# Kernel tuning notes

Measured on AMD Instinct MI355X. Metric: run time of the kernel, lower is better.

The kernel has to match this reference:

```python
import jax, jax.numpy as jnp
import numpy as np

B, S, D, H = 4, 2048, 1024, 16
DK = D // H

def setup_inputs() -> dict:
    key = jax.random.key(0)
    ks = jax.random.split(key, 5)
    scale = D ** -0.5  # keep activations well-scaled for random weights
    return {
        "x": jax.random.normal(ks[0], (B, S, D), dtype=jnp.float32),
        "w_q": jax.random.normal(ks[1], (D, D), dtype=jnp.float32) * scale,
        "w_k": jax.random.normal(ks[2], (D, D), dtype=jnp.float32) * scale,
        "w_v": jax.random.normal(ks[3], (D, D), dtype=jnp.float32) * scale,
        "w_o": jax.random.normal(ks[4], (D, D), dtype=jnp.float32) * scale,
        "b_o": jnp.zeros((D,), dtype=jnp.float32),
    }

def reference(x, w_q, w_k, w_v, w_o, b_o):
    b, s, d = x.shape
    # nn.Linear applies x @ W^T; project then split heads -> [b, h, s, dk]
    q = (x @ w_q.T).reshape(b, s, H, DK).transpose(0, 2, 1, 3)
    k = (x @ w_k.T).reshape(b, s, H, DK).transpose(0, 2, 1, 3)
    v = (x @ w_v.T).reshape(b, s, H, DK).transpose(0, 2, 1, 3)
    scores = jnp.einsum('bhqd,bhkd->bhqk', q, k) * (DK ** -0.5)
    causal = jnp.tril(jnp.ones((s, s), dtype=bool))  # [s, s]
    scores = jnp.where(causal, scores, jnp.float32(-1e9))
    attn = jax.nn.softmax(scores, axis=-1)
    out = jnp.einsum('bhqk,bhkd->bhqd', attn, v)
    out = out.transpose(0, 2, 1, 3).reshape(b, s, d)
    return out @ w_o.T + b_o
```

## Files before the change

### kernel.cpp

```cpp
#include <hip/hip_runtime.h>

typedef unsigned short u16;
typedef unsigned int u32;
typedef __attribute__((ext_vector_type(4))) u16 u16x4;
typedef __attribute__((ext_vector_type(8))) short short8;
typedef __attribute__((ext_vector_type(4))) float f32x4;
typedef __attribute__((ext_vector_type(16))) float f32x16;
typedef __attribute__((ext_vector_type(4))) u32 uint4v;

#define AS1 __attribute__((address_space(1)))
#define AS3 __attribute__((address_space(3)))

#define B_  4
#define S_  2048
#define D_  1024
#define H_  16
#define DK_ 64

#define WAIT_VM(n) asm volatile("s_waitcnt vmcnt(" #n ")" ::: "memory")
#define WAIT_LGK0  asm volatile("s_waitcnt lgkmcnt(0)" ::: "memory")

__device__ __forceinline__ u16 f2bf(float f) {
  union { float f; unsigned u; } v; v.f = f;
  unsigned r = v.u + 0x7fffu + ((v.u >> 16) & 1u);
  return (u16)(r >> 16);
}

__device__ __forceinline__ u32 cvt_pk_bf16(float lo, float hi) {
  u32 r;
  asm("v_cvt_pk_bf16_f32 %0, %1, %2" : "=v"(r) : "v"(lo), "v"(hi));
  return r;
}

__device__ __forceinline__ void pl32_swap(u32& a, u32& b) {
  asm("v_permlane32_swap_b32 %0, %1" : "+v"(a), "+v"(b));
}

__device__ __forceinline__ void gload_lds16(const void* g, void* l) {
  __builtin_amdgcn_global_load_lds((const AS1 void*)g, (AS3 void*)l, 16, 0, 0);
}

__global__ __launch_bounds__(256) void conv_bf16(const float* __restrict__ in,
                                                 u16* __restrict__ out,
                                                 int n, float scale) {
  int i = (blockIdx.x * 256 + threadIdx.x) * 8;
  if (i >= n) return;
  f32x4 a = *reinterpret_cast<const f32x4*>(in + i);
  f32x4 b = *reinterpret_cast<const f32x4*>(in + i + 4);
  union { u16 u[8]; uint4v v; } r;
#pragma unroll
  for (int j = 0; j < 4; ++j) {
    r.u[j]     = f2bf(a[j] * scale);
    r.u[4 + j] = f2bf(b[j] * scale);
  }
  *reinterpret_cast<uint4v*>(out + i) = r.v;
}

__global__ __launch_bounds__(256) void conv_w4(const float* __restrict__ w0,
                                               const float* __restrict__ w1,
                                               const float* __restrict__ w2,
                                               const float* __restrict__ w3,
                                               u16* __restrict__ out, float s0) {
  int y = blockIdx.y;
  const float* src = (y == 0) ? w0 : (y == 1) ? w1 : (y == 2) ? w2 : w3;
  float scale = (y == 0) ? s0 : 1.0f;
  int i = (blockIdx.x * 256 + threadIdx.x) * 8;
  f32x4 a = *reinterpret_cast<const f32x4*>(src + i);
  f32x4 b = *reinterpret_cast<const f32x4*>(src + i + 4);
  union { u16 u[8]; uint4v v; } r;
#pragma unroll
  for (int j = 0; j < 4; ++j) {
    r.u[j]     = f2bf(a[j] * scale);
    r.u[4 + j] = f2bf(b[j] * scale);
  }
  *reinterpret_cast<uint4v*>(out + (size_t)y * (D_ * D_) + i) = r.v;
}

template<int MODE>
__global__ __launch_bounds__(256) void gemm_bt(const u16* __restrict__ A,
                                               const u16* __restrict__ B,
                                               u16* __restrict__ Qb,
                                               u16* __restrict__ Kb,
                                               u16* __restrict__ Vt,
                                               float* __restrict__ Cf,
                                               const float* __restrict__ bias,
                                               int M, int N, int K, int nbx) {
  __shared__ __attribute__((aligned(16))) u16 As[2][128 * 64];
  __shared__ __attribute__((aligned(16))) u16 Bs[2][128 * 64];

  const int t = threadIdx.x;
  const int l = t & 63;
  const int w = t >> 6;
  const int wr = w >> 1, wc = w & 1;
  const int dd = blockIdx.x;
  const int cpx = gridDim.x >> 3;
  const int lid = (dd & 7) * cpx + (dd >> 3);
  const int m0 = (lid / nbx) * 128;
  const int n0 = (lid % nbx) * 128;
  const int NT = K >> 6;

  f32x4 zero = {0.f, 0.f, 0.f, 0.f};
  f32x4 acc[4][4];
#pragma unroll
  for (int i = 0; i < 4; ++i)
#pragma unroll
    for (int j = 0; j < 4; ++j) acc[i][j] = zero;

  auto stage = [&](int kt, int buf) {
#pragma unroll
    for (int i = 0; i < 4; ++i) {
      int slot = i * 256 + t;
      int r = slot >> 3, c = slot & 7;
      gload_lds16(A + (size_t)(m0 + r) * K + kt * 64 + ((c ^ (r & 7)) * 8),
                  (char*)&As[buf][0] + (size_t)(i * 256 + w * 64) * 16);
      gload_lds16(B + (size_t)(n0 + r) * K + kt * 64 + ((c ^ (r & 7)) * 8),
                  (char*)&Bs[buf][0] + (size_t)(i * 256 + w * 64) * 16);
    }
  };

  stage(0, 0);
  stage(1, 1);

  for (int kt = 0; kt < NT; ++kt) {
    const int buf = kt & 1;
    if (kt < NT - 1) { WAIT_VM(8); } else { WAIT_VM(0); }
    __builtin_amdgcn_s_barrier();
    __builtin_amdgcn_sched_barrier(0);

#pragma unroll
    for (int kc = 0; kc < 2; ++kc) {
      short8 a[4], bf[4];
      int lc = kc * 4 + (l >> 4);
#pragma unroll
      for (int i = 0; i < 4; ++i) {
        int ra = wr * 64 + i * 16 + (l & 15);
        a[i] = *reinterpret_cast<const short8*>(&As[buf][ra * 64 + ((lc ^ (ra & 7)) * 8)]);
        int rb = wc * 64 + i * 16 + (l & 15);
        bf[i] = *reinterpret_cast<const short8*>(&Bs[buf][rb * 64 + ((lc ^ (rb & 7)) * 8)]);
      }
#pragma unroll
      for (int mi = 0; mi < 4; ++mi)
#pragma unroll
        for (int ni = 0; ni < 4; ++ni)
          acc[mi][ni] = __builtin_amdgcn_mfma_f32_16x16x32_bf16(a[mi], bf[ni], acc[mi][ni], 0, 0, 0);
    }

    WAIT_LGK0;
    __builtin_amdgcn_sched_barrier(0);
    __builtin_amdgcn_s_barrier();
    if (kt + 2 < NT) stage(kt + 2, buf);
  }

#pragma unroll
  for (int ni = 0; ni < 4; ++ni) {
    int col = n0 + wc * 64 + ni * 16 + (l & 15);
    float bv = (MODE == 1) ? bias[col] : 0.f;
#pragma unroll
    for (int mi = 0; mi < 4; ++mi) {
      int row0 = m0 + wr * 64 + mi * 16 + (l >> 4) * 4;
      if (MODE == 1) {
#pragma unroll
        for (int r = 0; r < 4; ++r)
          Cf[(size_t)(row0 + r) * N + col] = acc[mi][ni][r] + bv;
      } else {
        if (col < 2048) {
          u16* dst = (col < 1024) ? Qb : Kb;
          int c = col & 1023;
#pragma unroll
          for (int r = 0; r < 4; ++r)
            dst[(size_t)(row0 + r) * 1024 + c] = f2bf(acc[mi][ni][r]);
        } else {
          int vc = col - 2048;
          int bh = (row0 >> 11) * 16 + (vc >> 6);
          int s0 = row0 & 2047;
          u16x4 pk;
#pragma unroll
          for (int r = 0; r < 4; ++r) pk[r] = f2bf(acc[mi][ni][r]);
          *reinterpret_cast<u16x4*>(Vt + ((size_t)(bh * 64 + (vc & 63))) * 2048 + s0) = pk;
        }
      }
    }
  }
}

__global__ __launch_bounds__(512) void attn_fwd(const u16* __restrict__ Q,
                                                const u16* __restrict__ K,
                                                const u16* __restrict__ Vtg,
                                                u16* __restrict__ AO) {
  __shared__ __attribute__((aligned(16))) u16 smem[24576];
  u16* Ksb = smem;
  u16* Vsb = smem + 12288;

  const int t = threadIdx.x;
  const int l = t & 63;
  const int w = t >> 6;
  const int hi = l >> 5;
  const int hi8 = hi * 8, hi4 = hi * 4;
  const int bh = blockIdx.x;
  const int by = blockIdx.y;
  const int s = (by < 4) ? (7 - 2 * by) : (2 * (by - 4));
  const size_t qkbase = (size_t)((bh >> 4) * S_) * D_ + (bh & 15) * DK_;
  const u16* Vg = Vtg + (size_t)bh * 64 * S_;

  const int qw = s * 256 + w * 32;
  const int qi = qw + (l & 31);

  short8 qf[4];
#pragma unroll
  for (int c = 0; c < 4; ++c)
    qf[c] = *reinterpret_cast<const short8*>(Q + qkbase + (size_t)qi * D_ + c * 16 + hi8);

  f32x16 o0 = {0,0,0,0,0,0,0,0,0,0,0,0,0,0,0,0};
  f32x16 o1 = {0,0,0,0,0,0,0,0,0,0,0,0,0,0,0,0};
  float l_r = 0.f;

  const int nst = 4 * (s + 1);

  auto stage = [&](int jt, u16* kdst, u16* vdst) {
    const u16* Ksrc = K + qkbase + (size_t)(jt * 64) * D_;
    const u16* Vsrc = Vg + jt * 64;
    int r = t >> 3, c = t & 7;
    gload_lds16(Ksrc + (size_t)r * D_ + ((c ^ (r & 7)) * 8),
                (char*)kdst + (size_t)t * 16);
    gload_lds16(Vsrc + (size_t)r * S_ + ((c ^ (r & 7)) * 8),
                (char*)vdst + (size_t)t * 16);
  };

  stage(0, Ksb, Vsb);
  stage(1, Ksb + 4096, Vsb + 4096);
  stage(2, Ksb + 8192, Vsb + 8192);
  int o0b = 0, o1b = 4096, o2b = 8192;

  for (int it = 0; it < nst; ++it) {
    if (it < nst - 2)       { WAIT_VM(4); }
    else if (it == nst - 2) { WAIT_VM(2); }
    else                    { WAIT_VM(0); }
    __builtin_amdgcn_s_barrier();
    __builtin_amdgcn_sched_barrier(0);

    const int j0 = it * 64;
    u16* ks = Ksb + o0b;
    u16* vs = Vsb + o0b;

    if (j0 <= qw + 31) {
      f32x16 s0 = {0,0,0,0,0,0,0,0,0,0,0,0,0,0,0,0};
      f32x16 s1 = {0,0,0,0,0,0,0,0,0,0,0,0,0,0,0,0};
#pragma unroll
      for (int c = 0; c < 4; ++c) {
        int cl = 2 * c + hi;
        int k0r = l & 31, k1r = (l & 31) + 32;
        short8 kf0 = *reinterpret_cast<const short8*>(&ks[k0r * 64 + ((cl ^ (k0r & 7)) * 8)]);
        short8 kf1 = *reinterpret_cast<const short8*>(&ks[k1r * 64 + ((cl ^ (k1r & 7)) * 8)]);
        s0 = __builtin_amdgcn_mfma_f32_32x32x16_bf16(kf0, qf[c], s0, 0, 0, 0);
        s1 = __builtin_amdgcn_mfma_f32_32x32x16_bf16(kf1, qf[c], s1, 0, 0, 0);
      }
      if (j0 + 63 > qw) {
#pragma unroll
        for (int r = 0; r < 16; ++r) {
          int key = j0 + (r & 3) + 8 * (r >> 2) + hi4;
          if (key > qi) s0[r] = -INFINITY;
          if (key + 32 > qi) s1[r] = -INFINITY;
        }
      }
      {
        float sum = 0.f;
#pragma unroll
        for (int r = 0; r < 16; ++r) { s0[r] = exp2f(s0[r]); sum += s0[r]; }
#pragma unroll
        for (int r = 0; r < 16; ++r) { s1[r] = exp2f(s1[r]); sum += s1[r]; }
        sum += __shfl_xor(sum, 32);
        l_r += sum;
      }
#pragma unroll
      for (int ksl = 0; ksl < 4; ++ksl) {
        const int b = 8 * (ksl & 1);
        const f32x16& ps = (ksl < 2) ? s0 : s1;
        u32 c0 = cvt_pk_bf16(ps[b + 0], ps[b + 1]);
        u32 c1 = cvt_pk_bf16(ps[b + 2], ps[b + 3]);
        u32 c2 = cvt_pk_bf16(ps[b + 4], ps[b + 5]);
        u32 c3 = cvt_pk_bf16(ps[b + 6], ps[b + 7]);
        pl32_swap(c0, c2);
        pl32_swap(c1, c3);
        union { u32 u[4]; short8 s; } pa;
        pa.u[0] = c0; pa.u[1] = c1; pa.u[2] = c2; pa.u[3] = c3;
        int cl = 2 * ksl + hi;
        int d0r = l & 31, d1r = (l & 31) + 32;
        short8 vf0 = *reinterpret_cast<const short8*>(&vs[d0r * 64 + ((cl ^ (d0r & 7)) * 8)]);
        short8 vf1 = *reinterpret_cast<const short8*>(&vs[d1r * 64 + ((cl ^ (d1r & 7)) * 8)]);
        o0 = __builtin_amdgcn_mfma_f32_32x32x16_bf16(vf0, pa.s, o0, 0, 0, 0);
        o1 = __builtin_amdgcn_mfma_f32_32x32x16_bf16(vf1, pa.s, o1, 0, 0, 0);
      }
    }

    WAIT_LGK0;
    __builtin_amdgcn_sched_barrier(0);
    __builtin_amdgcn_s_barrier();
    if (it + 3 < nst) stage(it + 3, Ksb + o0b, Vsb + o0b);
    int tmp = o0b; o0b = o1b; o1b = o2b; o2b = tmp;
  }

  float inv = 1.0f / l_r;
  u16* Ob = smem + w * 2304;
#pragma unroll
  for (int acc = 0; acc < 2; ++acc) {
    const f32x16& oo = acc ? o1 : o0;
#pragma unroll
    for (int rp = 0; rp < 8; ++rp) {
      u32 pk = cvt_pk_bf16(oo[2 * rp] * inv, oo[2 * rp + 1] * inv);
      int d0 = ((2 * rp) & 3) + 8 * (rp >> 1) + hi4 + 32 * acc;
      *reinterpret_cast<u32*>(&Ob[(l & 31) * 72 + d0]) = pk;
    }
  }
  __syncthreads();
  int qq = l >> 1;
  int chb = (l & 1) * 4;
#pragma unroll
  for (int c2 = 0; c2 < 4; ++c2) {
    uint4v vv = *reinterpret_cast<const uint4v*>(&Ob[qq * 72 + (chb + c2) * 8]);
    *reinterpret_cast<uint4v*>(&AO[qkbase + (size_t)(qw + qq) * D_ + (chb + c2) * 8]) = vv;
  }
}

extern "C" void kernel_launch(void* const* d_in, const int* in_sizes, int n_in,
                              void* d_out, int out_size, void* d_ws, size_t ws_size,
                              hipStream_t stream) {
  const float* x  = (const float*)d_in[0];
  const float* wq = (const float*)d_in[1];
  const float* wk = (const float*)d_in[2];
  const float* wv = (const float*)d_in[3];
  const float* wo = (const float*)d_in[4];
  const float* bo = (const float*)d_in[5];
  float* out = (float*)d_out;

  char* ws = (char*)d_ws;
  u16* XB   = (u16*)(ws);
  u16* WQKV = (u16*)(ws + (size_t)(16 << 20));
  u16* WOB  = (u16*)(ws + (size_t)(22 << 20));
  u16* Qb   = (u16*)(ws + (size_t)(24 << 20));
  u16* Kb   = (u16*)(ws + (size_t)(40 << 20));
  u16* Vt   = (u16*)(ws + (size_t)(56 << 20));
  u16* AO   = (u16*)(ws + (size_t)(72 << 20));

  const int nx = B_ * S_ * D_;
  const int nw = D_ * D_;

  conv_bf16<<<nx / 2048, 256, 0, stream>>>(x, XB, nx, 1.0f);
  conv_w4<<<dim3(nw / 2048, 4), 256, 0, stream>>>(wq, wk, wv, wo, WQKV,
                                                  0.18033688011112042f);

  gemm_bt<0><<<1536, 256, 0, stream>>>(
      XB, WQKV, Qb, Kb, Vt, nullptr, nullptr, B_ * S_, 3072, D_, 24);

  attn_fwd<<<dim3(B_ * H_, 8), 512, 0, stream>>>(Qb, Kb, Vt, AO);

  gemm_bt<1><<<512, 256, 0, stream>>>(
      AO, WOB, nullptr, nullptr, nullptr, out, bo, B_ * S_, D_, D_, 8);
}
```

Measured before the change: 163.3 us.

## Use 256x256 tiles with 512 threads for the QKV projection GEMM

Splits the shared GEMM template into a dedicated QKV kernel and an output-projection kernel. The QKV kernel now uses 256x256 block tiles, 8 waves each computing a 128x64 sub-tile, and a double-buffered pipeline that prefetches one step ahead instead of two, launched as 384 blocks. Larger tiles raise arithmetic intensity and cut redundant global loads of A and B. The costs are 128KB of LDS per block, a larger accumulator register footprint, fewer blocks than the 256 CUs can balance evenly, and a shallower prefetch that may expose load latency.

Measured after the change: 177.0 us. +8.4%, slower.

```diff
diff --git a/kernel.cpp b/kernel.cpp
--- a/kernel.cpp
+++ b/kernel.cpp
@@ -76,12 +76,104 @@
   *reinterpret_cast<uint4v*>(out + (size_t)y * (D_ * D_) + i) = r.v;
 }
 
-template<int MODE>
-__global__ __launch_bounds__(256) void gemm_bt(const u16* __restrict__ A,
+__global__ __launch_bounds__(512, 2) void gemm_qkv(const u16* __restrict__ A,
+                                                   const u16* __restrict__ B,
+                                                   u16* __restrict__ Qb,
+                                                   u16* __restrict__ Kb,
+                                                   u16* __restrict__ Vt,
+                                                   int M, int N, int K, int nbx) {
+  __shared__ __attribute__((aligned(16))) u16 As[2][256 * 64];
+  __shared__ __attribute__((aligned(16))) u16 Bs[2][256 * 64];
+
+  const int t = threadIdx.x;
+  const int l = t & 63;
+  const int w = t >> 6;
+  const int wm = w >> 2;
+  const int wn = w & 3;
+  const int dd = blockIdx.x;
+  const int cpx = gridDim.x >> 3;
+  const int lid = (dd & 7) * cpx + (dd >> 3);
+  const int m0 = (lid / nbx) * 256;
+  const int n0 = (lid % nbx) * 256;
+  const int NT = K >> 6;
+
+  f32x4 zero = {0.f, 0.f, 0.f, 0.f};
+  f32x4 acc[8][4];
+#pragma unroll
+  for (int i = 0; i < 8; ++i)
+#pragma unroll
+    for (int j = 0; j < 4; ++j) acc[i][j] = zero;
+
+  auto stage = [&](int kt, int buf) {
+#pragma unroll
+    for (int i = 0; i < 4; ++i) {
+      int slot = i * 512 + t;
+      int r = slot >> 3, c = slot & 7;
+      gload_lds16(A + (size_t)(m0 + r) * K + kt * 64 + ((c ^ (r & 7)) * 8),
+                  (char*)&As[buf][0] + (size_t)(i * 512 + w * 64) * 16);
+      gload_lds16(B + (size_t)(n0 + r) * K + kt * 64 + ((c ^ (r & 7)) * 8),
+                  (char*)&Bs[buf][0] + (size_t)(i * 512 + w * 64) * 16);
+    }
+  };
+
+  stage(0, 0);
+
+  for (int kt = 0; kt < NT; ++kt) {
+    const int buf = kt & 1;
+    WAIT_VM(0);
+    __builtin_amdgcn_s_barrier();
+    __builtin_amdgcn_sched_barrier(0);
+    if (kt + 1 < NT) stage(kt + 1, buf ^ 1);
+
+#pragma unroll
+    for (int kc = 0; kc < 2; ++kc) {
+      short8 a[8], bfr[4];
+      int lc = kc * 4 + (l >> 4);
+#pragma unroll
+      for (int i = 0; i < 8; ++i) {
+        int ra = wm * 128 + i * 16 + (l & 15);
+        a[i] = *reinterpret_cast<const short8*>(&As[buf][ra * 64 + ((lc ^ (ra & 7)) * 8)]);
+      }
+#pragma unroll
+      for (int i = 0; i < 4; ++i) {
+        int rb = wn * 64 + i * 16 + (l & 15);
+        bfr[i] = *reinterpret_cast<const short8*>(&Bs[buf][rb * 64 + ((lc ^ (rb & 7)) * 8)]);
+      }
+#pragma unroll
+      for (int mi = 0; mi < 8; ++mi)
+#pragma unroll
+        for (int ni = 0; ni < 4; ++ni)
+          acc[mi][ni] = __builtin_amdgcn_mfma_f32_16x16x32_bf16(a[mi], bfr[ni], acc[mi][ni], 0, 0, 0);
+    }
+  }
+
+#pragma unroll
+  for (int ni = 0; ni < 4; ++ni) {
+    int col = n0 + wn * 64 + ni * 16 + (l & 15);
+#pragma unroll
+    for (int mi = 0; mi < 8; ++mi) {
+      int row0 = m0 + wm * 128 + mi * 16 + (l >> 4) * 4;
+      if (col < 2048) {
+        u16* dst = (col < 1024) ? Qb : Kb;
+        int c = col & 1023;
+#pragma unroll
+        for (int r = 0; r < 4; ++r)
+          dst[(size_t)(row0 + r) * 1024 + c] = f2bf(acc[mi][ni][r]);
+      } else {
+        int vc = col - 2048;
+        int bh = (row0 >> 11) * 16 + (vc >> 6);
+        int s0 = row0 & 2047;
+        u16x4 pk;
+#pragma unroll
+        for (int r = 0; r < 4; ++r) pk[r] = f2bf(acc[mi][ni][r]);
+        *reinterpret_cast<u16x4*>(Vt + ((size_t)(bh * 64 + (vc & 63))) * 2048 + s0) = pk;
+      }
+    }
+  }
+}
+
+__global__ __launch_bounds__(256) void gemm_op(const u16* __restrict__ A,
                                                const u16* __restrict__ B,
-                                               u16* __restrict__ Qb,
-                                               u16* __restrict__ Kb,
-                                               u16* __restrict__ Vt,
                                                float* __restrict__ Cf,
                                                const float* __restrict__ bias,
                                                int M, int N, int K, int nbx) {
@@ -154,31 +246,13 @@
 #pragma unroll
   for (int ni = 0; ni < 4; ++ni) {
     int col = n0 + wc * 64 + ni * 16 + (l & 15);
-    float bv = (MODE == 1) ? bias[col] : 0.f;
+    float bv = bias[col];
 #pragma unroll
     for (int mi = 0; mi < 4; ++mi) {
       int row0 = m0 + wr * 64 + mi * 16 + (l >> 4) * 4;
-      if (MODE == 1) {
-#pragma unroll
-        for (int r = 0; r < 4; ++r)
-          Cf[(size_t)(row0 + r) * N + col] = acc[mi][ni][r] + bv;
-      } else {
-        if (col < 2048) {
-          u16* dst = (col < 1024) ? Qb : Kb;
-          int c = col & 1023;
-#pragma unroll
-          for (int r = 0; r < 4; ++r)
-            dst[(size_t)(row0 + r) * 1024 + c] = f2bf(acc[mi][ni][r]);
-        } else {
-          int vc = col - 2048;
-          int bh = (row0 >> 11) * 16 + (vc >> 6);
-          int s0 = row0 & 2047;
-          u16x4 pk;
-#pragma unroll
-          for (int r = 0; r < 4; ++r) pk[r] = f2bf(acc[mi][ni][r]);
-          *reinterpret_cast<u16x4*>(Vt + ((size_t)(bh * 64 + (vc & 63))) * 2048 + s0) = pk;
-        }
-      }
+#pragma unroll
+      for (int r = 0; r < 4; ++r)
+        Cf[(size_t)(row0 + r) * N + col] = acc[mi][ni][r] + bv;
     }
   }
 }
@@ -348,11 +422,11 @@
   conv_w4<<<dim3(nw / 2048, 4), 256, 0, stream>>>(wq, wk, wv, wo, WQKV,
                                                   0.18033688011112042f);
 
-  gemm_bt<0><<<1536, 256, 0, stream>>>(
-      XB, WQKV, Qb, Kb, Vt, nullptr, nullptr, B_ * S_, 3072, D_, 24);
+  gemm_qkv<<<384, 512, 0, stream>>>(
+      XB, WQKV, Qb, Kb, Vt, B_ * S_, 3072, D_, 12);
 
   attn_fwd<<<dim3(B_ * H_, 8), 512, 0, stream>>>(Qb, Kb, Vt, AO);
 
-  gemm_bt<1><<<512, 256, 0, stream>>>(
-      AO, WOB, nullptr, nullptr, nullptr, out, bo, B_ * S_, D_, D_, 8);
-}
+  gemm_op<<<512, 256, 0, stream>>>(
+      AO, WOB, out, bo, B_ * S_, D_, D_, 8);
+}
```
